# Kernel optimization log

Hardware: AMD Instinct MI355X
Metric: run time of the kernel (lower is better)

The kernel has to match this reference:

```python
import jax, jax.numpy as jnp
import numpy as np
import math

ROPE_THETA = 10000.0


def apply_rope(x, positions):
    # x: [B, H, S, d_k], positions: [S]
    d_k = x.shape[-1]
    inv_freq = 1.0 / (ROPE_THETA ** (jnp.arange(0, d_k, 2, dtype=jnp.float32) / d_k))  # [d_k/2]
    angles = positions.astype(jnp.float32)[:, None] * inv_freq[None, :]  # [S, d_k/2]
    cos = jnp.cos(angles)
    sin = jnp.sin(angles)
    x1 = x[..., 0::2]
    x2 = x[..., 1::2]
    r1 = x1 * cos - x2 * sin
    r2 = x1 * sin + x2 * cos
    out = jnp.stack([r1, r2], axis=-1)  # interleave pairs back
    return out.reshape(x.shape)


def setup_inputs() -> dict:
    key = jax.random.key(0)
    k1, k2, k3 = jax.random.split(key, 3)
    B, S, D = 4, 2048, 1024
    x = jax.random.normal(k1, (B, S, D), dtype=jnp.float32)
    token_positions = jnp.arange(S, dtype=jnp.int32)
    w_qkv = jax.random.normal(k2, (3 * D, D), dtype=jnp.float32) * (1.0 / math.sqrt(D))
    w_o = jax.random.normal(k3, (D, D), dtype=jnp.float32) * (1.0 / math.sqrt(D))
    return {"x": x, "token_positions": token_positions, "w_qkv": w_qkv, "w_o": w_o}


def reference(x, token_positions, w_qkv, w_o):
    B, S, D = x.shape
    H = 16
    d_k = D // H
    qkv = jnp.einsum('bsd,ed->bse', x, w_qkv)  # [B, S, 3D]
    # rearrange '... s (stack h dk) -> stack ... h s dk'
    qkv = qkv.reshape(B, S, 3, H, d_k)
    q = jnp.transpose(qkv[:, :, 0], (0, 2, 1, 3))  # [B, H, S, dk]
    k = jnp.transpose(qkv[:, :, 1], (0, 2, 1, 3))
    v = jnp.transpose(qkv[:, :, 2], (0, 2, 1, 3))
    q = apply_rope(q, token_positions)
    k = apply_rope(k, token_positions)
    scores = jnp.einsum('bhqd,bhkd->bhqk', q, k) / math.sqrt(d_k)
    causal = jnp.tril(jnp.ones((S, S), dtype=bool))
    scores = jnp.where(causal[None, None], scores, -jnp.inf)
    attn = jax.nn.softmax(scores, axis=-1)
    out = jnp.einsum('bhqk,bhkd->bhqd', attn, v)  # [B, H, S, dk]
    out = jnp.transpose(out, (0, 2, 1, 3)).reshape(B, S, D)
    return jnp.einsum('bsd,ed->bse', out, w_o)
```

## Files before the change

kernel.cpp:

```cpp
#include <hip/hip_runtime.h>
#include <hip/hip_bf16.h>
#include <math.h>

typedef __bf16 bf16_t;
typedef __attribute__((ext_vector_type(8))) __bf16 bf16x8;
typedef __attribute__((ext_vector_type(4))) __bf16 bf16x4;
typedef __attribute__((ext_vector_type(4))) float f32x4;

#define MFMA_16x16x32(A_, B_, C_) __builtin_amdgcn_mfma_f32_16x16x32_bf16((A_), (B_), (C_), 0, 0, 0)

#define Bsz 4
#define Ssz 2048
#define Dsz 1024
#define Hh 16
#define DKd 64
#define Mrows (Bsz * Ssz)
#define N1 (3 * Dsz)
#define KD Dsz

__global__ void cvt_f32_bf16_kernel(const float* __restrict__ src, bf16_t* __restrict__ dst, int n4) {
  int i = blockIdx.x * blockDim.x + threadIdx.x;
  if (i >= n4) return;
  float4 v = reinterpret_cast<const float4*>(src)[i];
  bf16x4 o = {(bf16_t)v.x, (bf16_t)v.y, (bf16_t)v.z, (bf16_t)v.w};
  reinterpret_cast<bf16x4*>(dst)[i] = o;
}

__global__ void rope_tab_kernel(const int* __restrict__ pos, float2* __restrict__ tab) {
  int i = blockIdx.x * blockDim.x + threadIdx.x;
  if (i >= Ssz * 32) return;
  int s = i >> 5, f = i & 31;
  float inv_freq = powf(10000.0f, -(float)(2 * f) / 64.0f);
  float a = (float)pos[s] * inv_freq;
  tab[i] = make_float2(cosf(a), sinf(a));
}

__global__ __launch_bounds__(512, 2) void gemm256_qkv_kernel(
    const bf16_t* __restrict__ A, const bf16_t* __restrict__ Bt,
    bf16_t* __restrict__ qb, bf16_t* __restrict__ kb, bf16_t* __restrict__ vtb,
    const float2* __restrict__ tab) {
  constexpr int NT = KD / 64;
  __shared__ __align__(16) bf16_t As[2][256 * 64];
  __shared__ __align__(16) bf16_t Bs[2][192 * 64];
  const int t = threadIdx.x;
  const int w = t >> 6, l = t & 63;
  const int lr = l & 15, lk = l >> 4;
  const int rs = lr >> 1;
  const int wm = w >> 2, wn = w & 3;
  const int m0 = blockIdx.y * 256, n0 = blockIdx.x * 192;

  const int gcol = ((t & 7) ^ ((t >> 4) & 7)) * 8;
  const bf16_t* gA = A + (size_t)(m0 + (t >> 3)) * KD + gcol;
  const bf16_t* gB = Bt + (size_t)(n0 + (t >> 3)) * KD + gcol;

  f32x4 acc[8][3] = {};

#define QSTAGE(PH, KT)                                                                 \
  do {                                                                                 \
    _Pragma("unroll") for (int i = 0; i < 4; ++i)                                      \
        __builtin_amdgcn_global_load_lds(gA + (size_t)i * 64 * KD + (KT),              \
                                         &As[PH][(i * 64 + w * 8) * 64], 16, 0, 0);    \
    _Pragma("unroll") for (int i = 0; i < 3; ++i)                                      \
        __builtin_amdgcn_global_load_lds(gB + (size_t)i * 64 * KD + (KT),              \
                                         &Bs[PH][(i * 64 + w * 8) * 64], 16, 0, 0);    \
  } while (0)

  QSTAGE(0, 0);
  __syncthreads();
  for (int tt = 0; tt < NT; ++tt) {
    const int b = tt & 1;
    if (tt + 1 < NT) QSTAGE(b ^ 1, (tt + 1) * 64);
    bf16x8 bfv[3][2];
#pragma unroll
    for (int n = 0; n < 3; ++n) {
      const int R = wn * 48 + n * 16 + lr;
#pragma unroll
      for (int ks = 0; ks < 2; ++ks)
        bfv[n][ks] = *reinterpret_cast<const bf16x8*>(&Bs[b][R * 64 + (((ks * 4 + lk) ^ rs) * 8)]);
    }
#pragma unroll
    for (int mp = 0; mp < 4; ++mp) {
      bf16x8 af[2][2];
#pragma unroll
      for (int mi = 0; mi < 2; ++mi) {
        const int R = wm * 128 + (mp * 2 + mi) * 16 + lr;
#pragma unroll
        for (int ks = 0; ks < 2; ++ks)
          af[mi][ks] = *reinterpret_cast<const bf16x8*>(&As[b][R * 64 + (((ks * 4 + lk) ^ rs) * 8)]);
      }
      __builtin_amdgcn_s_setprio(1);
#pragma unroll
      for (int mi = 0; mi < 2; ++mi)
#pragma unroll
        for (int n = 0; n < 3; ++n) {
          acc[mp * 2 + mi][n] = MFMA_16x16x32(af[mi][0], bfv[n][0], acc[mp * 2 + mi][n]);
          acc[mp * 2 + mi][n] = MFMA_16x16x32(af[mi][1], bfv[n][1], acc[mp * 2 + mi][n]);
        }
      __builtin_amdgcn_s_setprio(0);
    }
    __syncthreads();
  }
#undef QSTAGE

#pragma unroll
  for (int n = 0; n < 3; ++n) {
    const int colbase = n0 + wn * 48 + n * 16;
    const int sect = colbase >> 10;
    const int h = (colbase >> 6) & 15;
    const int dk = (colbase & 63) + lr;
    if (sect < 2) {
      bf16_t* dst0 = (sect == 0) ? qb : kb;
#pragma unroll
      for (int m = 0; m < 8; ++m)
#pragma unroll
        for (int r = 0; r < 4; ++r) {
          const int grow = m0 + wm * 128 + m * 16 + lk * 4 + r;
          const int bb = grow >> 11, s = grow & (Ssz - 1);
          const float v = acc[m][n][r];
          const float pv = __shfl_xor(v, 1);
          const float2 cs = tab[(s << 5) | (dk >> 1)];
          float vr = (dk & 1) ? (pv * cs.y + v * cs.x) : (v * cs.x - pv * cs.y);
          if (sect == 0) vr *= 0.125f;
          dst0[((size_t)(bb * Hh + h) * Ssz + s) * DKd + dk] = (bf16_t)vr;
        }
    } else {
#pragma unroll
      for (int m = 0; m < 8; ++m)
#pragma unroll
        for (int r = 0; r < 4; ++r) {
          const int grow = m0 + wm * 128 + m * 16 + lk * 4 + r;
          const int bb = grow >> 11, s = grow & (Ssz - 1);
          vtb[((size_t)(bb * Hh + h) * DKd + dk) * Ssz + s] = (bf16_t)acc[m][n][r];
        }
    }
  }
}

__global__ __launch_bounds__(512, 2) void gemm_out_kernel(
    const bf16_t* __restrict__ A, const bf16_t* __restrict__ Bt,
    float* __restrict__ fout) {
  constexpr int NT = KD / 64;
  __shared__ __align__(16) bf16_t As[2][256 * 64];
  __shared__ __align__(16) bf16_t Bs[2][128 * 64];
  const int t = threadIdx.x;
  const int w = t >> 6, l = t & 63;
  const int lr = l & 15, lk = l >> 4;
  const int rs = lr >> 1;
  const int wm = w >> 2, wn = w & 3;
  const int m0 = blockIdx.y * 256, n0 = blockIdx.x * 128;

  const int gcol = ((t & 7) ^ ((t >> 4) & 7)) * 8;
  const bf16_t* gA = A + (size_t)(m0 + (t >> 3)) * KD + gcol;
  const bf16_t* gB = Bt + (size_t)(n0 + (t >> 3)) * KD + gcol;

  f32x4 acc[8][2] = {};

#define OSTAGE(PH, KT)                                                                 \
  do {                                                                                 \
    _Pragma("unroll") for (int i = 0; i < 4; ++i)                                      \
        __builtin_amdgcn_global_load_lds(gA + (size_t)i * 64 * KD + (KT),              \
                                         &As[PH][(i * 64 + w * 8) * 64], 16, 0, 0);    \
    _Pragma("unroll") for (int i = 0; i < 2; ++i)                                      \
        __builtin_amdgcn_global_load_lds(gB + (size_t)i * 64 * KD + (KT),              \
                                         &Bs[PH][(i * 64 + w * 8) * 64], 16, 0, 0);    \
  } while (0)

  OSTAGE(0, 0);
  __syncthreads();
  for (int tt = 0; tt < NT; ++tt) {
    const int b = tt & 1;
    if (tt + 1 < NT) OSTAGE(b ^ 1, (tt + 1) * 64);
    bf16x8 bfv[2][2];
#pragma unroll
    for (int n = 0; n < 2; ++n) {
      const int R = wn * 32 + n * 16 + lr;
#pragma unroll
      for (int ks = 0; ks < 2; ++ks)
        bfv[n][ks] = *reinterpret_cast<const bf16x8*>(&Bs[b][R * 64 + (((ks * 4 + lk) ^ rs) * 8)]);
    }
#pragma unroll
    for (int mp = 0; mp < 4; ++mp) {
      bf16x8 af[2][2];
#pragma unroll
      for (int mi = 0; mi < 2; ++mi) {
        const int R = wm * 128 + (mp * 2 + mi) * 16 + lr;
#pragma unroll
        for (int ks = 0; ks < 2; ++ks)
          af[mi][ks] = *reinterpret_cast<const bf16x8*>(&As[b][R * 64 + (((ks * 4 + lk) ^ rs) * 8)]);
      }
      __builtin_amdgcn_s_setprio(1);
#pragma unroll
      for (int mi = 0; mi < 2; ++mi)
#pragma unroll
        for (int n = 0; n < 2; ++n) {
          acc[mp * 2 + mi][n] = MFMA_16x16x32(af[mi][0], bfv[n][0], acc[mp * 2 + mi][n]);
          acc[mp * 2 + mi][n] = MFMA_16x16x32(af[mi][1], bfv[n][1], acc[mp * 2 + mi][n]);
        }
      __builtin_amdgcn_s_setprio(0);
    }
    __syncthreads();
  }
#undef OSTAGE

#pragma unroll
  for (int m = 0; m < 8; ++m)
#pragma unroll
    for (int r = 0; r < 4; ++r) {
      const int grow = m0 + wm * 128 + m * 16 + lk * 4 + r;
      float* op = fout + (size_t)grow * Dsz + n0 + wn * 32 + lr;
      op[0] = acc[m][0][r];
      op[16] = acc[m][1][r];
    }
}

__global__ __launch_bounds__(256, 3) void attn_kernel(
    const bf16_t* __restrict__ qb, const bf16_t* __restrict__ kb,
    const bf16_t* __restrict__ vtb, bf16_t* __restrict__ aout) {
  __shared__ __align__(16) bf16_t Ks[64 * 64];
  __shared__ __align__(16) bf16_t Vs[64 * 64];
  const int t = threadIdx.x, w = t >> 6, l = t & 63;
  const int lr = l & 15, lk = l >> 4;
  const int bid = blockIdx.x;
  const int bh = (bid & 7) * 8 + ((bid >> 3) & 7);
  const int qt = 15 - (bid >> 6);
  const int q0 = qt * 128;
  const int sub0 = q0 + w * 32;

  const bf16_t* qbase = qb + ((size_t)bh * Ssz + sub0) * DKd;
  bf16x8 qf[2][2];
#pragma unroll
  for (int s = 0; s < 2; ++s) {
    qf[s][0] = *reinterpret_cast<const bf16x8*>(qbase + (s * 16 + lr) * DKd + lk * 8);
    qf[s][1] = *reinterpret_cast<const bf16x8*>(qbase + (s * 16 + lr) * DKd + 32 + lk * 8);
  }

  f32x4 o[2][4] = {};
  float mrow[2] = {-INFINITY, -INFINITY};
  float lsum[2] = {0.f, 0.f};

  const int srow = t >> 2;
  const int scc = (t & 3) * 2;
  const bf16_t* kg = kb + ((size_t)bh * Ssz + srow) * DKd + scc * 8;
  const bf16_t* vg = vtb + ((size_t)bh * DKd + srow) * Ssz + scc * 8;
  bf16_t* ksw0 = Ks + srow * 64 + ((scc ^ (srow & 7)) * 8);
  bf16_t* ksw1 = Ks + srow * 64 + (((scc + 1) ^ (srow & 7)) * 8);
  bf16_t* vw[4];
#pragma unroll
  for (int u = 0; u < 2; ++u) {
    const int c = scc + u;
    const int B = 32 * (c >> 2) + 16 * (c & 1) + 4 * ((c & 3) >> 1);
    const int ch = B >> 3, off = B & 7;
    vw[2 * u] = Vs + srow * 64 + ((ch ^ (srow & 7)) * 8) + off;
    vw[2 * u + 1] = Vs + srow * 64 + (((ch + 1) ^ (srow & 7)) * 8) + off;
  }

  const int kvend = q0 + 128;
  bf16x8 pk0 = *reinterpret_cast<const bf16x8*>(kg);
  bf16x8 pk1 = *reinterpret_cast<const bf16x8*>(kg + 8);
  bf16x8 pv0 = *reinterpret_cast<const bf16x8*>(vg);
  bf16x8 pv1 = *reinterpret_cast<const bf16x8*>(vg + 8);

  for (int kv = 0; kv < kvend; kv += 64) {
    __syncthreads();
    *reinterpret_cast<bf16x8*>(ksw0) = pk0;
    *reinterpret_cast<bf16x8*>(ksw1) = pk1;
    *reinterpret_cast<bf16x4*>(vw[0]) = __builtin_shufflevector(pv0, pv0, 0, 1, 2, 3);
    *reinterpret_cast<bf16x4*>(vw[1]) = __builtin_shufflevector(pv0, pv0, 4, 5, 6, 7);
    *reinterpret_cast<bf16x4*>(vw[2]) = __builtin_shufflevector(pv1, pv1, 0, 1, 2, 3);
    *reinterpret_cast<bf16x4*>(vw[3]) = __builtin_shufflevector(pv1, pv1, 4, 5, 6, 7);
    __syncthreads();
    if (kv + 64 < kvend) {
      pk0 = *reinterpret_cast<const bf16x8*>(kg + (size_t)(kv + 64) * DKd);
      pk1 = *reinterpret_cast<const bf16x8*>(kg + (size_t)(kv + 64) * DKd + 8);
      pv0 = *reinterpret_cast<const bf16x8*>(vg + kv + 64);
      pv1 = *reinterpret_cast<const bf16x8*>(vg + kv + 64 + 8);
    }
#pragma unroll
    for (int s = 0; s < 2; ++s) {
      const int subrow = sub0 + s * 16;
      if (kv > subrow + 15) continue;
      f32x4 sa[4];
#pragma unroll
      for (int n = 0; n < 4; ++n) {
        const int R = n * 16 + lr;
        const bf16x8 a0 = *reinterpret_cast<const bf16x8*>(Ks + R * 64 + ((lk ^ (R & 7)) * 8));
        const bf16x8 a1 = *reinterpret_cast<const bf16x8*>(Ks + R * 64 + (((lk + 4) ^ (R & 7)) * 8));
        f32x4 z = {};
        z = MFMA_16x16x32(a0, qf[s][0], z);
        z = MFMA_16x16x32(a1, qf[s][1], z);
        sa[n] = z;
      }
      if (kv + 63 > subrow) {
        const int qrow = subrow + lr;
        const int kbase = kv + lk * 4;
#pragma unroll
        for (int n = 0; n < 4; ++n)
#pragma unroll
          for (int r = 0; r < 4; ++r)
            if (kbase + n * 16 + r > qrow) sa[n][r] = -INFINITY;
      }
      float mx = fmaxf(fmaxf(fmaxf(sa[0][0], sa[0][1]), fmaxf(sa[0][2], sa[0][3])),
                       fmaxf(fmaxf(sa[1][0], sa[1][1]), fmaxf(sa[1][2], sa[1][3])));
      mx = fmaxf(mx, fmaxf(fmaxf(fmaxf(sa[2][0], sa[2][1]), fmaxf(sa[2][2], sa[2][3])),
                           fmaxf(fmaxf(sa[3][0], sa[3][1]), fmaxf(sa[3][2], sa[3][3]))));
      mx = fmaxf(mx, __shfl_xor(mx, 16));
      mx = fmaxf(mx, __shfl_xor(mx, 32));
      const float mnew = fmaxf(mrow[s], mx);
      const float scl = __expf(mrow[s] - mnew);
      mrow[s] = mnew;
      float ps = 0.f;
#pragma unroll
      for (int n = 0; n < 4; ++n)
#pragma unroll
        for (int r = 0; r < 4; ++r) {
          const float p = __expf(sa[n][r] - mnew);
          sa[n][r] = p;
          ps += p;
        }
      lsum[s] = lsum[s] * scl + ps;
#pragma unroll
      for (int n = 0; n < 4; ++n)
#pragma unroll
        for (int r = 0; r < 4; ++r) o[s][n][r] *= scl;
      bf16x8 pb0, pb1;
#pragma unroll
      for (int r = 0; r < 4; ++r) {
        pb0[r] = (bf16_t)sa[0][r];
        pb0[4 + r] = (bf16_t)sa[1][r];
        pb1[r] = (bf16_t)sa[2][r];
        pb1[4 + r] = (bf16_t)sa[3][r];
      }
#pragma unroll
      for (int n = 0; n < 4; ++n) {
        const int R = n * 16 + lr;
        const bf16x8 v0 = *reinterpret_cast<const bf16x8*>(Vs + R * 64 + ((lk ^ (R & 7)) * 8));
        const bf16x8 v1 = *reinterpret_cast<const bf16x8*>(Vs + R * 64 + (((lk + 4) ^ (R & 7)) * 8));
        o[s][n] = MFMA_16x16x32(v0, pb0, o[s][n]);
        o[s][n] = MFMA_16x16x32(v1, pb1, o[s][n]);
      }
    }
  }
  const int b_ = bh >> 4, h_ = bh & 15;
#pragma unroll
  for (int s = 0; s < 2; ++s) {
    float sm = lsum[s];
    sm += __shfl_xor(sm, 16);
    sm += __shfl_xor(sm, 32);
    const float inv = 1.0f / sm;
    const int qrow = sub0 + s * 16 + lr;
    bf16_t* op = aout + ((size_t)b_ * Ssz + qrow) * Dsz + h_ * DKd + lk * 4;
#pragma unroll
    for (int n = 0; n < 4; ++n) {
      const bf16x4 ov = {(bf16_t)(o[s][n][0] * inv), (bf16_t)(o[s][n][1] * inv),
                         (bf16_t)(o[s][n][2] * inv), (bf16_t)(o[s][n][3] * inv)};
      *reinterpret_cast<bf16x4*>(op + n * 16) = ov;
    }
  }
}

extern "C" void kernel_launch(void* const* d_in, const int* in_sizes, int n_in,
                              void* d_out, int out_size, void* d_ws, size_t ws_size,
                              hipStream_t stream) {
  const float* x = (const float*)d_in[0];
  const int* pos = (const int*)d_in[1];
  const float* wqkv = (const float*)d_in[2];
  const float* wo = (const float*)d_in[3];
  float* out = (float*)d_out;

  bf16_t* xb = (bf16_t*)d_ws;
  bf16_t* wqkvb = xb + (size_t)Mrows * KD;
  bf16_t* wob = wqkvb + (size_t)N1 * KD;
  bf16_t* qbuf = wob + (size_t)Dsz * KD;
  bf16_t* kbuf = qbuf + (size_t)64 * Ssz * DKd;
  bf16_t* vtb = kbuf + (size_t)64 * Ssz * DKd;
  float2* tab = (float2*)(vtb + (size_t)64 * Ssz * DKd);
  bf16_t* aout = xb;

  {
    int n4 = Mrows * KD / 4;
    cvt_f32_bf16_kernel<<<(n4 + 255) / 256, 256, 0, stream>>>(x, xb, n4);
  }
  {
    int n4 = N1 * KD / 4;
    cvt_f32_bf16_kernel<<<(n4 + 255) / 256, 256, 0, stream>>>(wqkv, wqkvb, n4);
  }
  {
    int n4 = Dsz * KD / 4;
    cvt_f32_bf16_kernel<<<(n4 + 255) / 256, 256, 0, stream>>>(wo, wob, n4);
  }
  rope_tab_kernel<<<(Ssz * 32 + 255) / 256, 256, 0, stream>>>(pos, tab);

  gemm256_qkv_kernel<<<dim3(N1 / 192, Mrows / 256), 512, 0, stream>>>(
      xb, wqkvb, qbuf, kbuf, vtb, tab);

  attn_kernel<<<dim3(16 * 64), 256, 0, stream>>>(qbuf, kbuf, vtb, aout);

  gemm_out_kernel<<<dim3(Dsz / 128, Mrows / 256), 512, 0, stream>>>(
      aout, wob, out);
}
```

Measured before the change: 187.4 us.

## Interleave QKV GEMM prefetch loads with MFMA phases and vectorize V-transpose stores

Measured after the change: 179.0 us. 1.05x faster.

```diff
diff --git a/kernel.cpp b/kernel.cpp
--- a/kernel.cpp
+++ b/kernel.cpp
@@ -35,7 +35,7 @@
   tab[i] = make_float2(cosf(a), sinf(a));
 }
 
-__global__ __launch_bounds__(512, 2) void gemm256_qkv_kernel(
+__global__ __launch_bounds__(512, 1) void gemm256_qkv_kernel(
     const bf16_t* __restrict__ A, const bf16_t* __restrict__ Bt,
     bf16_t* __restrict__ qb, bf16_t* __restrict__ kb, bf16_t* __restrict__ vtb,
     const float2* __restrict__ tab) {
@@ -54,53 +54,81 @@
   const bf16_t* gB = Bt + (size_t)(n0 + (t >> 3)) * KD + gcol;
 
   f32x4 acc[8][3] = {};
-
-#define QSTAGE(PH, KT)                                                                 \
-  do {                                                                                 \
-    _Pragma("unroll") for (int i = 0; i < 4; ++i)                                      \
-        __builtin_amdgcn_global_load_lds(gA + (size_t)i * 64 * KD + (KT),              \
-                                         &As[PH][(i * 64 + w * 8) * 64], 16, 0, 0);    \
-    _Pragma("unroll") for (int i = 0; i < 3; ++i)                                      \
-        __builtin_amdgcn_global_load_lds(gB + (size_t)i * 64 * KD + (KT),              \
-                                         &Bs[PH][(i * 64 + w * 8) * 64], 16, 0, 0);    \
+  bf16x8 bfv[3][2];
+
+#define LDA_(I_, SB_, KT_)                                                        \
+  __builtin_amdgcn_global_load_lds(gA + (size_t)(I_) * 64 * KD + (KT_),           \
+                                   &As[SB_][((I_) * 64 + w * 8) * 64], 16, 0, 0)
+#define LDB_(I_, SB_, KT_)                                                        \
+  __builtin_amdgcn_global_load_lds(gB + (size_t)(I_) * 64 * KD + (KT_),           \
+                                   &Bs[SB_][((I_) * 64 + w * 8) * 64], 16, 0, 0)
+
+#define PH(BUF_, P_, STG0_, STG1_, VMW_)                                          \
+  do {                                                                            \
+    if ((P_) == 0) {                                                              \
+      _Pragma("unroll") for (int n_ = 0; n_ < 3; ++n_) {                          \
+        const int R_ = wn * 48 + n_ * 16 + lr;                                    \
+        bfv[n_][0] = *reinterpret_cast<const bf16x8*>(                            \
+            &Bs[BUF_][R_ * 64 + ((lk ^ rs) * 8)]);                                \
+        bfv[n_][1] = *reinterpret_cast<const bf16x8*>(                            \
+            &Bs[BUF_][R_ * 64 + (((4 + lk) ^ rs) * 8)]);                          \
+      }                                                                           \
+    }                                                                             \
+    bf16x8 af0_[2], af1_[2];                                                      \
+    {                                                                             \
+      const int Ra_ = wm * 128 + (P_) * 32 + lr;                                  \
+      const int Rb_ = Ra_ + 16;                                                   \
+      af0_[0] = *reinterpret_cast<const bf16x8*>(&As[BUF_][Ra_ * 64 + ((lk ^ rs) * 8)]);       \
+      af0_[1] = *reinterpret_cast<const bf16x8*>(&As[BUF_][Ra_ * 64 + (((4 + lk) ^ rs) * 8)]); \
+      af1_[0] = *reinterpret_cast<const bf16x8*>(&As[BUF_][Rb_ * 64 + ((lk ^ rs) * 8)]);       \
+      af1_[1] = *reinterpret_cast<const bf16x8*>(&As[BUF_][Rb_ * 64 + (((4 + lk) ^ rs) * 8)]); \
+    }                                                                             \
+    STG0_;                                                                        \
+    STG1_;                                                                        \
+    __builtin_amdgcn_s_barrier();                                                 \
+    asm volatile("s_waitcnt lgkmcnt(0)" ::: "memory");                            \
+    __builtin_amdgcn_sched_barrier(0);                                            \
+    __builtin_amdgcn_s_setprio(1);                                                \
+    _Pragma("unroll") for (int n_ = 0; n_ < 3; ++n_) {                            \
+      acc[(P_)*2][n_] = MFMA_16x16x32(af0_[0], bfv[n_][0], acc[(P_)*2][n_]);      \
+      acc[(P_)*2][n_] = MFMA_16x16x32(af0_[1], bfv[n_][1], acc[(P_)*2][n_]);      \
+      acc[(P_)*2 + 1][n_] = MFMA_16x16x32(af1_[0], bfv[n_][0], acc[(P_)*2 + 1][n_]); \
+      acc[(P_)*2 + 1][n_] = MFMA_16x16x32(af1_[1], bfv[n_][1], acc[(P_)*2 + 1][n_]); \
+    }                                                                             \
+    __builtin_amdgcn_s_setprio(0);                                                \
+    VMW_;                                                                         \
+    __builtin_amdgcn_s_barrier();                                                 \
   } while (0)
 
-  QSTAGE(0, 0);
-  __syncthreads();
-  for (int tt = 0; tt < NT; ++tt) {
-    const int b = tt & 1;
-    if (tt + 1 < NT) QSTAGE(b ^ 1, (tt + 1) * 64);
-    bf16x8 bfv[3][2];
-#pragma unroll
-    for (int n = 0; n < 3; ++n) {
-      const int R = wn * 48 + n * 16 + lr;
-#pragma unroll
-      for (int ks = 0; ks < 2; ++ks)
-        bfv[n][ks] = *reinterpret_cast<const bf16x8*>(&Bs[b][R * 64 + (((ks * 4 + lk) ^ rs) * 8)]);
-    }
-#pragma unroll
-    for (int mp = 0; mp < 4; ++mp) {
-      bf16x8 af[2][2];
-#pragma unroll
-      for (int mi = 0; mi < 2; ++mi) {
-        const int R = wm * 128 + (mp * 2 + mi) * 16 + lr;
-#pragma unroll
-        for (int ks = 0; ks < 2; ++ks)
-          af[mi][ks] = *reinterpret_cast<const bf16x8*>(&As[b][R * 64 + (((ks * 4 + lk) ^ rs) * 8)]);
-      }
-      __builtin_amdgcn_s_setprio(1);
-#pragma unroll
-      for (int mi = 0; mi < 2; ++mi)
-#pragma unroll
-        for (int n = 0; n < 3; ++n) {
-          acc[mp * 2 + mi][n] = MFMA_16x16x32(af[mi][0], bfv[n][0], acc[mp * 2 + mi][n]);
-          acc[mp * 2 + mi][n] = MFMA_16x16x32(af[mi][1], bfv[n][1], acc[mp * 2 + mi][n]);
-        }
-      __builtin_amdgcn_s_setprio(0);
-    }
-    __syncthreads();
-  }
-#undef QSTAGE
+#define VM4_ do { asm volatile("s_waitcnt vmcnt(4)" ::: "memory"); __builtin_amdgcn_sched_barrier(0); } while (0)
+#define VM2_ do { asm volatile("s_waitcnt vmcnt(2)" ::: "memory"); __builtin_amdgcn_sched_barrier(0); } while (0)
+
+#define TILE_(BUF_, KTN_)                                                         \
+  do {                                                                            \
+    PH(BUF_, 0, LDB_(0, (BUF_) ^ 1, KTN_), LDB_(1, (BUF_) ^ 1, KTN_), (void)0);   \
+    PH(BUF_, 1, LDB_(2, (BUF_) ^ 1, KTN_), LDA_(0, (BUF_) ^ 1, KTN_), VM4_);      \
+    PH(BUF_, 2, LDA_(2, (BUF_) ^ 1, KTN_), LDA_(1, (BUF_) ^ 1, KTN_), (void)0);   \
+    PH(BUF_, 3, LDA_(3, (BUF_) ^ 1, KTN_), (void)0, VM2_);                        \
+  } while (0)
+
+  LDB_(0, 0, 0); LDB_(1, 0, 0); LDB_(2, 0, 0);
+  LDA_(0, 0, 0); LDA_(2, 0, 0); LDA_(1, 0, 0); LDA_(3, 0, 0);
+  asm volatile("s_waitcnt vmcnt(2)" ::: "memory");
+  __builtin_amdgcn_s_barrier();
+
+#pragma unroll 1
+  for (int tt = 0; tt < NT; tt += 2) {
+    const int ktn0 = ((tt + 1) & (NT - 1)) * 64;
+    TILE_(0, ktn0);
+    const int ktn1 = ((tt + 2) & (NT - 1)) * 64;
+    TILE_(1, ktn1);
+  }
+#undef TILE_
+#undef VM4_
+#undef VM2_
+#undef PH
+#undef LDA_
+#undef LDB_
 
 #pragma unroll
   for (int n = 0; n < 3; ++n) {
@@ -125,13 +153,14 @@
         }
     } else {
 #pragma unroll
-      for (int m = 0; m < 8; ++m)
-#pragma unroll
-        for (int r = 0; r < 4; ++r) {
-          const int grow = m0 + wm * 128 + m * 16 + lk * 4 + r;
-          const int bb = grow >> 11, s = grow & (Ssz - 1);
-          vtb[((size_t)(bb * Hh + h) * DKd + dk) * Ssz + s] = (bf16_t)acc[m][n][r];
-        }
+      for (int m = 0; m < 8; ++m) {
+        const int grow0 = m0 + wm * 128 + m * 16 + lk * 4;
+        const int bb = grow0 >> 11, s0 = grow0 & (Ssz - 1);
+        const bf16x4 ov = {(bf16_t)acc[m][n][0], (bf16_t)acc[m][n][1],
+                           (bf16_t)acc[m][n][2], (bf16_t)acc[m][n][3]};
+        *reinterpret_cast<bf16x4*>(
+            vtb + ((size_t)(bb * Hh + h) * DKd + dk) * Ssz + s0) = ov;
+      }
     }
   }
 }
```
